# Kernel tuning notes

Measured on AMD Instinct MI355X. Metric: run time of the kernel, lower is better.

## Reference

```python
import jax, jax.numpy as jnp
import numpy as np

BS, C_IN, L = 64, 64, 4096
C_OUT, KS, K, RATIO = 128, 7, 4, 4
HIDDEN = C_IN // RATIO
PAD, TEMP = 3, 30.0


def setup_inputs() -> dict:
    key = jax.random.key(0)
    k1, k2, k3, k4, k5 = jax.random.split(key, 5)
    x = jax.random.normal(k1, (BS, C_IN, L), dtype=jnp.float32)
    # attention 1x1 convs stored as matmul matrices
    w_attn1 = jax.random.normal(k2, (HIDDEN, C_IN), dtype=jnp.float32) * (2.0 / C_IN) ** 0.5
    w_attn2 = jax.random.normal(k3, (K, HIDDEN), dtype=jnp.float32) * (2.0 / HIDDEN) ** 0.5
    # K-bank conv weights [K, out, in, ks] and biases [K, out]
    weight = jax.random.normal(k4, (K, C_OUT, C_IN, KS), dtype=jnp.float32) * 0.05
    bias = jax.random.normal(k5, (K, C_OUT), dtype=jnp.float32) * 0.05
    return {"x": x, "w_attn1": w_attn1, "w_attn2": w_attn2, "weight": weight, "bias": bias}


def reference(x, w_attn1, w_attn2, weight, bias):
    # Attention1d: global avg pool -> 1x1 conv -> relu -> 1x1 conv -> softmax(./T)
    pooled = jnp.mean(x, axis=-1)                      # [bs, C_in]
    h = jax.nn.relu(pooled @ w_attn1.T)                # [bs, hidden]
    logits = h @ w_attn2.T                             # [bs, K]
    att = jax.nn.softmax(logits / TEMP, axis=-1)       # [bs, K]

    # softmax-weighted aggregation of the K weight banks -> per-sample kernels
    agg_w = jnp.einsum('bk,koif->boif', att, weight)   # [bs, out, in, ks]
    agg_b = att @ bias                                 # [bs, out]

    # per-sample conv1d (the grouped-conv trick), vectorized with vmap
    def conv_one(xi, wi):
        # xi: [C_in, L], wi: [out, in, ks]
        return jax.lax.conv_general_dilated(
            xi[None], wi, window_strides=(1,), padding=[(PAD, PAD)],
            dimension_numbers=('NCH', 'OIH', 'NCH'))[0]  # [out, L]

    out = jax.vmap(conv_one)(x, agg_w) + agg_b[:, :, None]  # [bs, out, L]
    return out
```

## Files before the change

### kernel.cpp

```cpp
#include <hip/hip_runtime.h>

typedef __bf16 bf16;
typedef __bf16 bf16x8 __attribute__((ext_vector_type(8)));
typedef __bf16 bf16x2 __attribute__((ext_vector_type(2)));
typedef float f32x4 __attribute__((ext_vector_type(4)));

#define BS 64
#define CI 64
#define LEN 4096
#define CO 128
#define KS 7
#define NK 4
#define HID 16
#define TEMP 30.0f

#define KTOT 448
#define WROW 456
#define WBAT (CO * WROW)
#define XROW 72
#define XC 134
#define LTILE 128

__global__ void pool_kernel(const float* __restrict__ x, float* __restrict__ pooled) {
    int bc = blockIdx.x;
    const float4* xp = (const float4*)(x + (size_t)bc * LEN);
    int t = threadIdx.x;
    float s = 0.f;
#pragma unroll
    for (int j = 0; j < 4; ++j) {
        float4 v = xp[t + 256 * j];
        s += (v.x + v.y) + (v.z + v.w);
    }
#pragma unroll
    for (int off = 32; off > 0; off >>= 1) s += __shfl_down(s, off, 64);
    __shared__ float red[4];
    if ((t & 63) == 0) red[t >> 6] = s;
    __syncthreads();
    if (t == 0) pooled[bc] = (red[0] + red[1] + red[2] + red[3]) * (1.0f / LEN);
}

__global__ void attn_kernel(const float* __restrict__ pooled,
                            const float* __restrict__ w1,
                            const float* __restrict__ w2,
                            const float* __restrict__ bias,
                            float* __restrict__ att_g,
                            float* __restrict__ aggb_g) {
    int b = blockIdx.x, t = threadIdx.x;
    __shared__ float p[CI], h[HID], att[NK];
    if (t < CI) p[t] = pooled[b * CI + t];
    __syncthreads();
    if (t < HID) {
        float s = 0.f;
        for (int i = 0; i < CI; ++i) s += p[i] * w1[t * CI + i];
        h[t] = fmaxf(s, 0.f);
    }
    __syncthreads();
    if (t == 0) {
        float lg[NK];
        float m = -1e30f;
        for (int k = 0; k < NK; ++k) {
            float s = 0.f;
            for (int j = 0; j < HID; ++j) s += h[j] * w2[k * HID + j];
            lg[k] = s * (1.0f / TEMP);
            m = fmaxf(m, lg[k]);
        }
        float e[NK], tot = 0.f;
        for (int k = 0; k < NK; ++k) { e[k] = expf(lg[k] - m); tot += e[k]; }
        float inv = 1.0f / tot;
        for (int k = 0; k < NK; ++k) { att[k] = e[k] * inv; att_g[b * NK + k] = att[k]; }
    }
    __syncthreads();
    if (t < CO) {
        float s = 0.f;
        for (int k = 0; k < NK; ++k) s += att[k] * bias[k * CO + t];
        aggb_g[b * CO + t] = s;
    }
}

__global__ void aggw_kernel(const float* __restrict__ weight,
                            const float* __restrict__ att_g,
                            bf16* __restrict__ wagg) {
    int o = blockIdx.x >> 1;
    int bh = blockIdx.x & 1;
    int t = threadIdx.x;
    __shared__ float lw[4 * KTOT];
    __shared__ __align__(16) float attl[128];

    const float* wo = weight + o * KTOT;
    for (int idx = t; idx < 4 * KTOT; idx += 256) {
        int bank = idx / KTOT;
        int r = idx - bank * KTOT;
        lw[idx] = wo[(size_t)bank * (CO * KTOT) + r];
    }
    if (t < 128) attl[t] = att_g[bh * 128 + t];
    __syncthreads();

    if (t < 224) {
        float w8[8];
#pragma unroll
        for (int j = 0; j < 2; ++j) {
            int kout = 2 * t + j;
            int i = kout & 63, f = kout >> 6;
#pragma unroll
            for (int bank = 0; bank < 4; ++bank)
                w8[j * 4 + bank] = lw[bank * KTOT + i * KS + f];
        }
        for (int bb = 0; bb < 32; ++bb) {
            int b = bh * 32 + bb;
            float4 a = *(const float4*)&attl[bb * 4];
            float v0 = a.x * w8[0] + a.y * w8[1] + a.z * w8[2] + a.w * w8[3];
            float v1 = a.x * w8[4] + a.y * w8[5] + a.z * w8[6] + a.w * w8[7];
            bf16x2 pk; pk[0] = (bf16)v0; pk[1] = (bf16)v1;
            *(bf16x2*)(wagg + (size_t)b * WBAT + o * WROW + 2 * t) = pk;
        }
    }
}

struct XStage { float4 m[8]; float e1, e2; };

__global__ __launch_bounds__(256, 2) void conv_kernel(
    const float* __restrict__ x,
    const bf16* __restrict__ wagg,
    const float* __restrict__ aggb,
    float* __restrict__ out) {
    __shared__ __align__(16) bf16 lds_x[XC * XROW];

    int nwg = gridDim.x;
    int bid = blockIdx.x;
    int logical = (bid & 7) * (nwg >> 3) + (bid >> 3);
    int b = logical >> 6;
    int lsp = (logical >> 1) & 31;
    int oh = logical & 1;

    int t = threadIdx.x;
    int lane = t & 63, wid = t >> 6;
    int ln = lane & 15, g = lane >> 4;
    int wm = wid >> 1, wn = wid & 1;

    const bf16* wgb = wagg + (size_t)b * WBAT
                    + (size_t)(oh * 64 + wm * 32 + ln) * WROW + g * 8;
    bf16x8 av[2][14];
#pragma unroll
    for (int mf = 0; mf < 2; ++mf)
#pragma unroll
        for (int kk = 0; kk < 14; ++kk)
            av[mf][kk] = *(const bf16x8*)(wgb + mf * 16 * WROW + kk * 32);

    int l0 = lsp * LTILE;
    int si = t >> 2, sf = t & 3;
    const float* xb = x + (size_t)b * CI * LEN;

    XStage s0;
#pragma unroll
    for (int j = 0; j < 8; ++j) {
        int c4 = sf + 4 * j;
        s0.m[j] = *(const float4*)(xb + (size_t)si * LEN + l0 + 4 * c4);
    }
    {
        int i1 = t / 6, s1 = t - i1 * 6;
        int c1 = (s1 < 3) ? s1 : (128 + s1);
        int gl1 = l0 - 3 + c1;
        s0.e1 = (gl1 >= 0 && gl1 < LEN) ? xb[(size_t)i1 * LEN + gl1] : 0.f;
        s0.e2 = 0.f;
        if (t < 128) {
            int e2 = 256 + t, i2 = e2 / 6, s2 = e2 - i2 * 6;
            int c2 = (s2 < 3) ? s2 : (128 + s2);
            int gl2 = l0 - 3 + c2;
            s0.e2 = (gl2 >= 0 && gl2 < LEN) ? xb[(size_t)i2 * LEN + gl2] : 0.f;
        }
    }

    float bias_r[2][4];
    int orow_off[2][4];
#pragma unroll
    for (int mf = 0; mf < 2; ++mf)
#pragma unroll
        for (int r = 0; r < 4; ++r) {
            int o = oh * 64 + wm * 32 + mf * 16 + g * 4 + r;
            bias_r[mf][r] = aggb[b * CO + o];
            orow_off[mf][r] = (b * CO + o) * LEN;
        }

#pragma unroll
    for (int j = 0; j < 8; ++j) {
        int c4 = sf + 4 * j;
#pragma unroll
        for (int dl = 0; dl < 4; ++dl) {
            float v = (&s0.m[j].x)[dl];
            lds_x[(4 * c4 + 3 + dl) * XROW + si] = (bf16)v;
        }
    }
    {
        int i1 = t / 6, s1 = t - i1 * 6;
        int c1 = (s1 < 3) ? s1 : (128 + s1);
        lds_x[c1 * XROW + i1] = (bf16)s0.e1;
        if (t < 128) {
            int e2 = 256 + t, i2 = e2 / 6, s2 = e2 - i2 * 6;
            int c2 = (s2 < 3) ? s2 : (128 + s2);
            lds_x[c2 * XROW + i2] = (bf16)s0.e2;
        }
    }
    __syncthreads();

    f32x4 acc[2][4];
#pragma unroll
    for (int mf = 0; mf < 2; ++mf)
#pragma unroll
        for (int nf = 0; nf < 4; ++nf)
            acc[mf][nf] = (f32x4){0.f, 0.f, 0.f, 0.f};

    const bf16* bp = lds_x + (wn * 64 + ln) * XROW + g * 8;

#pragma unroll
    for (int kk = 0; kk < 14; ++kk) {
        int boff = (kk >> 1) * XROW + (kk & 1) * 32;
        bf16x8 bv[4];
#pragma unroll
        for (int nf = 0; nf < 4; ++nf)
            bv[nf] = *(const bf16x8*)(bp + nf * 16 * XROW + boff);
#pragma unroll
        for (int mf = 0; mf < 2; ++mf)
#pragma unroll
            for (int nf = 0; nf < 4; ++nf)
                acc[mf][nf] = __builtin_amdgcn_mfma_f32_16x16x32_bf16(
                    av[mf][kk], bv[nf], acc[mf][nf], 0, 0, 0);
    }

#pragma unroll
    for (int mf = 0; mf < 2; ++mf)
#pragma unroll
        for (int nf = 0; nf < 4; ++nf) {
            int l = l0 + wn * 64 + nf * 16 + ln;
#pragma unroll
            for (int r = 0; r < 4; ++r)
                out[(size_t)orow_off[mf][r] + l] = acc[mf][nf][r] + bias_r[mf][r];
        }
}

extern "C" void kernel_launch(void* const* d_in, const int* in_sizes, int n_in,
                              void* d_out, int out_size, void* d_ws, size_t ws_size,
                              hipStream_t stream) {
    const float* x  = (const float*)d_in[0];
    const float* w1 = (const float*)d_in[1];
    const float* w2 = (const float*)d_in[2];
    const float* wt = (const float*)d_in[3];
    const float* bs = (const float*)d_in[4];
    float* out = (float*)d_out;

    bf16* wagg = (bf16*)d_ws;
    float* pooled = (float*)((char*)d_ws + (size_t)BS * WBAT * 2);
    float* att_g  = pooled + BS * CI;
    float* aggb   = att_g + BS * NK;

    pool_kernel<<<BS * CI, 256, 0, stream>>>(x, pooled);
    attn_kernel<<<BS, 256, 0, stream>>>(pooled, w1, w2, bs, att_g, aggb);
    aggw_kernel<<<CO * 2, 256, 0, stream>>>(wt, att_g, wagg);
    conv_kernel<<<BS * 64, 256, 0, stream>>>(x, wagg, aggb, out);
}
```

Measured before the change: 75.79 us.

## Loop conv blocks over multiple L tiles with double-buffered x and LDS-staged stores

Each conv workgroup now processes four consecutive 128-wide L tiles, so the per-sample weight fragments loaded into registers are reused across tiles and the grid shrinks fourfold. The next tile's x is prefetched into registers during the MFMA work and written to a second LDS buffer. Outputs are staged through per-wave LDS so each lane stores 16-byte vectors instead of scattered scalars. The cost is extra LDS use and fewer workgroups, which may reduce occupancy and latency hiding.

```diff
diff --git a/kernel.cpp b/kernel.cpp
--- a/kernel.cpp
+++ b/kernel.cpp
@@ -20,6 +20,8 @@
 #define XROW 72
 #define XC 134
 #define LTILE 128
+#define TPB 4
+#define WST 68
 
 __global__ void pool_kernel(const float* __restrict__ x, float* __restrict__ pooled) {
     int bc = blockIdx.x;
@@ -123,14 +125,15 @@
     const bf16* __restrict__ wagg,
     const float* __restrict__ aggb,
     float* __restrict__ out) {
-    __shared__ __align__(16) bf16 lds_x[XC * XROW];
+    __shared__ __align__(16) bf16 lds_x[2][XC * XROW];
+    __shared__ __align__(16) float lds_st[4][32 * WST];
 
     int nwg = gridDim.x;
     int bid = blockIdx.x;
     int logical = (bid & 7) * (nwg >> 3) + (bid >> 3);
-    int b = logical >> 6;
-    int lsp = (logical >> 1) & 31;
-    int oh = logical & 1;
+    int b = logical >> 4;
+    int rem = logical & 15;
+    int oh = rem >> 3, lsp = rem & 7;
 
     int t = threadIdx.x;
     int lane = t & 63, wid = t >> 6;
@@ -146,95 +149,113 @@
         for (int kk = 0; kk < 14; ++kk)
             av[mf][kk] = *(const bf16x8*)(wgb + mf * 16 * WROW + kk * 32);
 
-    int l0 = lsp * LTILE;
+    int l0base = lsp * (LTILE * TPB);
     int si = t >> 2, sf = t & 3;
     const float* xb = x + (size_t)b * CI * LEN;
 
-    XStage s0;
-#pragma unroll
-    for (int j = 0; j < 8; ++j) {
-        int c4 = sf + 4 * j;
-        s0.m[j] = *(const float4*)(xb + (size_t)si * LEN + l0 + 4 * c4);
-    }
-    {
+    auto load_x = [&](int l0, XStage& s) {
+#pragma unroll
+        for (int j = 0; j < 8; ++j) {
+            int c4 = sf + 4 * j;
+            s.m[j] = *(const float4*)(xb + (size_t)si * LEN + l0 + 4 * c4);
+        }
         int i1 = t / 6, s1 = t - i1 * 6;
         int c1 = (s1 < 3) ? s1 : (128 + s1);
         int gl1 = l0 - 3 + c1;
-        s0.e1 = (gl1 >= 0 && gl1 < LEN) ? xb[(size_t)i1 * LEN + gl1] : 0.f;
-        s0.e2 = 0.f;
+        s.e1 = (gl1 >= 0 && gl1 < LEN) ? xb[(size_t)i1 * LEN + gl1] : 0.f;
+        s.e2 = 0.f;
         if (t < 128) {
             int e2 = 256 + t, i2 = e2 / 6, s2 = e2 - i2 * 6;
             int c2 = (s2 < 3) ? s2 : (128 + s2);
             int gl2 = l0 - 3 + c2;
-            s0.e2 = (gl2 >= 0 && gl2 < LEN) ? xb[(size_t)i2 * LEN + gl2] : 0.f;
-        }
-    }
-
-    float bias_r[2][4];
-    int orow_off[2][4];
-#pragma unroll
-    for (int mf = 0; mf < 2; ++mf)
-#pragma unroll
-        for (int r = 0; r < 4; ++r) {
-            int o = oh * 64 + wm * 32 + mf * 16 + g * 4 + r;
-            bias_r[mf][r] = aggb[b * CO + o];
-            orow_off[mf][r] = (b * CO + o) * LEN;
-        }
-
-#pragma unroll
-    for (int j = 0; j < 8; ++j) {
-        int c4 = sf + 4 * j;
-#pragma unroll
-        for (int dl = 0; dl < 4; ++dl) {
-            float v = (&s0.m[j].x)[dl];
-            lds_x[(4 * c4 + 3 + dl) * XROW + si] = (bf16)v;
-        }
-    }
-    {
+            s.e2 = (gl2 >= 0 && gl2 < LEN) ? xb[(size_t)i2 * LEN + gl2] : 0.f;
+        }
+    };
+    auto write_x = [&](int buf, const XStage& s) {
+        bf16* lb = lds_x[buf];
+#pragma unroll
+        for (int j = 0; j < 8; ++j) {
+            int c4 = sf + 4 * j;
+#pragma unroll
+            for (int dl = 0; dl < 4; ++dl) {
+                float v = (&s.m[j].x)[dl];
+                lb[(4 * c4 + 3 + dl) * XROW + si] = (bf16)v;
+            }
+        }
         int i1 = t / 6, s1 = t - i1 * 6;
         int c1 = (s1 < 3) ? s1 : (128 + s1);
-        lds_x[c1 * XROW + i1] = (bf16)s0.e1;
+        lb[c1 * XROW + i1] = (bf16)s.e1;
         if (t < 128) {
             int e2 = 256 + t, i2 = e2 / 6, s2 = e2 - i2 * 6;
             int c2 = (s2 < 3) ? s2 : (128 + s2);
-            lds_x[c2 * XROW + i2] = (bf16)s0.e2;
-        }
-    }
-    __syncthreads();
-
-    f32x4 acc[2][4];
+            lb[c2 * XROW + i2] = (bf16)s.e2;
+        }
+    };
+
+    float bias_r[2][4];
 #pragma unroll
     for (int mf = 0; mf < 2; ++mf)
 #pragma unroll
-        for (int nf = 0; nf < 4; ++nf)
-            acc[mf][nf] = (f32x4){0.f, 0.f, 0.f, 0.f};
-
-    const bf16* bp = lds_x + (wn * 64 + ln) * XROW + g * 8;
-
-#pragma unroll
-    for (int kk = 0; kk < 14; ++kk) {
-        int boff = (kk >> 1) * XROW + (kk & 1) * 32;
-        bf16x8 bv[4];
-#pragma unroll
-        for (int nf = 0; nf < 4; ++nf)
-            bv[nf] = *(const bf16x8*)(bp + nf * 16 * XROW + boff);
+        for (int r = 0; r < 4; ++r)
+            bias_r[mf][r] = aggb[b * CO + oh * 64 + wm * 32 + mf * 16 + g * 4 + r];
+
+    XStage s0;
+    load_x(l0base, s0);
+    write_x(0, s0);
+    __syncthreads();
+
+    float* st = &lds_st[wid][0];
+    size_t orow0 = ((size_t)(b * CO + oh * 64 + wm * 32)) * LEN;
+
+    for (int tl = 0; tl < TPB; ++tl) {
+        int l0 = l0base + tl * LTILE;
+        XStage sn;
+        if (tl + 1 < TPB) load_x(l0 + LTILE, sn);
+
+        f32x4 acc[2][4];
 #pragma unroll
         for (int mf = 0; mf < 2; ++mf)
 #pragma unroll
             for (int nf = 0; nf < 4; ++nf)
-                acc[mf][nf] = __builtin_amdgcn_mfma_f32_16x16x32_bf16(
-                    av[mf][kk], bv[nf], acc[mf][nf], 0, 0, 0);
-    }
-
-#pragma unroll
-    for (int mf = 0; mf < 2; ++mf)
-#pragma unroll
-        for (int nf = 0; nf < 4; ++nf) {
-            int l = l0 + wn * 64 + nf * 16 + ln;
-#pragma unroll
-            for (int r = 0; r < 4; ++r)
-                out[(size_t)orow_off[mf][r] + l] = acc[mf][nf][r] + bias_r[mf][r];
-        }
+                acc[mf][nf] = (f32x4){0.f, 0.f, 0.f, 0.f};
+
+        const bf16* bp = lds_x[tl & 1] + (wn * 64 + ln) * XROW + g * 8;
+
+#pragma unroll
+        for (int kk = 0; kk < 14; ++kk) {
+            int boff = (kk >> 1) * XROW + (kk & 1) * 32;
+            bf16x8 bv[4];
+#pragma unroll
+            for (int nf = 0; nf < 4; ++nf)
+                bv[nf] = *(const bf16x8*)(bp + nf * 16 * XROW + boff);
+#pragma unroll
+            for (int mf = 0; mf < 2; ++mf)
+#pragma unroll
+                for (int nf = 0; nf < 4; ++nf)
+                    acc[mf][nf] = __builtin_amdgcn_mfma_f32_16x16x32_bf16(
+                        av[mf][kk], bv[nf], acc[mf][nf], 0, 0, 0);
+        }
+
+#pragma unroll
+        for (int mf = 0; mf < 2; ++mf)
+#pragma unroll
+            for (int nf = 0; nf < 4; ++nf)
+#pragma unroll
+                for (int r = 0; r < 4; ++r)
+                    st[(mf * 16 + g * 4 + r) * WST + nf * 16 + ln] =
+                        acc[mf][nf][r] + bias_r[mf][r];
+        asm volatile("s_waitcnt lgkmcnt(0)" ::: "memory");
+        __builtin_amdgcn_sched_barrier(0);
+#pragma unroll
+        for (int s = 0; s < 8; ++s) {
+            int rl = s * 4 + g;
+            f32x4 v = *(const f32x4*)(st + rl * WST + 4 * ln);
+            *(f32x4*)(out + orow0 + (size_t)rl * LEN + l0 + wn * 64 + 4 * ln) = v;
+        }
+
+        if (tl + 1 < TPB) write_x((tl + 1) & 1, sn);
+        if (tl + 1 < TPB) __syncthreads();
+    }
 }
 
 extern "C" void kernel_launch(void* const* d_in, const int* in_sizes, int n_in,
@@ -255,5 +276,5 @@
     pool_kernel<<<BS * CI, 256, 0, stream>>>(x, pooled);
     attn_kernel<<<BS, 256, 0, stream>>>(pooled, w1, w2, bs, att_g, aggb);
     aggw_kernel<<<CO * 2, 256, 0, stream>>>(wt, att_g, wagg);
-    conv_kernel<<<BS * 64, 256, 0, stream>>>(x, wagg, aggb, out);
-}
+    conv_kernel<<<BS * 16, 256, 0, stream>>>(x, wagg, aggb, out);
+}
```

Result: faster. 68.43 us (-9.7%).
